# Optimization experiments

Hardware: AMD Instinct MI355X
Metric: run time of the kernel (lower is better)

Reference implementation:

```python
import jax, jax.numpy as jnp
import numpy as np

N = 100000   # nodes
E = 1600000  # edges (avg degree 16)
B = 64       # graphs in batch
D_IN = 64
D = 64       # d_model


def setup_inputs() -> dict:
    key = jax.random.key(0)
    ks = jax.random.split(key, 12)
    inp = {}
    inp["x_raw"] = jax.random.normal(ks[0], (N, D_IN), dtype=jnp.float32)
    inp["edge_index"] = jax.random.randint(ks[1], (2, E), 0, N)
    inp["batch"] = jnp.sort(jax.random.randint(ks[2], (N,), 0, B))
    # SAGEConv params per layer: lin_l (weight+bias, applied to neighbor mean),
    # lin_r (weight only, applied to root) -- PyG defaults.
    dins = [D_IN, D, D]
    for i, din in enumerate(dins):
        scale = 1.0 / np.sqrt(din)
        inp[f"Wl{i}"] = jax.random.normal(ks[3 + 3 * i], (D, din), dtype=jnp.float32) * scale
        inp[f"bl{i}"] = jnp.zeros((D,), dtype=jnp.float32)
        inp[f"Wr{i}"] = jax.random.normal(ks[4 + 3 * i], (D, din), dtype=jnp.float32) * scale
    return inp


def _sage_conv(x, src, dst, Wl, bl, Wr):
    """PyG SAGEConv(normalize=True): mean-aggregate neighbors, lin_l + lin_r, L2 norm."""
    msg = jax.ops.segment_sum(x[src], dst, num_segments=N)          # [N, d_in]
    deg = jax.ops.segment_sum(jnp.ones((src.shape[0],), x.dtype), dst, num_segments=N)
    mean = msg / jnp.maximum(deg, 1.0)[:, None]
    out = mean @ Wl.T + bl + x @ Wr.T                               # [N, D]
    nrm = jnp.sqrt(jnp.sum(out * out, axis=-1, keepdims=True))
    return out / jnp.maximum(nrm, 1e-12)


def reference(x_raw, edge_index, batch, Wl0, bl0, Wr0, Wl1, bl1, Wr1, Wl2, bl2, Wr2):
    src, dst = edge_index[0], edge_index[1]
    # dropout is identity in eval mode
    h = jax.nn.relu(_sage_conv(x_raw, src, dst, Wl0, bl0, Wr0))
    h = jax.nn.relu(_sage_conv(h, src, dst, Wl1, bl1, Wr1))
    h = jax.nn.relu(_sage_conv(h, src, dst, Wl2, bl2, Wr2))
    # readout='sum': scatter-sum over batch ids -> [B, D]
    return jax.ops.segment_sum(h, batch, num_segments=B)
```

## Files before the change

kernel.cpp:

```cpp
#include <hip/hip_runtime.h>

#define DFEAT 64

typedef __attribute__((ext_vector_type(8))) short bf16x8;
typedef __attribute__((ext_vector_type(4))) float f32x4;

__device__ __forceinline__ float bfhi(unsigned int u) {
    return __builtin_bit_cast(float, u & 0xFFFF0000u);
}
__device__ __forceinline__ float bflo(unsigned int u) {
    return __builtin_bit_cast(float, u << 16);
}
__device__ __forceinline__ unsigned short f2bf(float f) {
    unsigned int u = __builtin_bit_cast(unsigned int, f);
    u += 0x7FFFu + ((u >> 16) & 1u);
    return (unsigned short)(u >> 16);
}
__device__ __forceinline__ float4 upk4(uint2 v) {
    float4 r;
    r.x = bflo(v.x); r.y = bfhi(v.x);
    r.z = bflo(v.y); r.w = bfhi(v.y);
    return r;
}

__global__ void __launch_bounds__(256)
cvt_bf16_kernel(const float* __restrict__ in, unsigned short* __restrict__ outb,
                int n4) {
    int i = blockIdx.x * 256 + threadIdx.x;
    if (i >= n4) return;
    const float4 v = reinterpret_cast<const float4*>(in)[i];
    uint2 p;
    p.x = (unsigned int)f2bf(v.x) | ((unsigned int)f2bf(v.y) << 16);
    p.y = (unsigned int)f2bf(v.z) | ((unsigned int)f2bf(v.w) << 16);
    reinterpret_cast<uint2*>(outb)[i] = p;
}


__global__ void __launch_bounds__(256)
bucket_hist_kernel(const int* __restrict__ dsts, int* __restrict__ bhist, int E) {
    __shared__ int h[512];
    const int tid = threadIdx.x;
    h[tid] = 0; h[tid + 256] = 0;
    __syncthreads();
    for (int e = blockIdx.x * 256 + tid; e < E; e += gridDim.x * 256)
        atomicAdd(&h[dsts[e] >> 8], 1);
    __syncthreads();
    for (int b = tid; b < 512; b += 256)
        if (h[b]) atomicAdd(&bhist[b], h[b]);
}

__global__ void __launch_bounds__(256)
bucket_scan_kernel(const int* __restrict__ bhist, int* __restrict__ bbase,
                   int* __restrict__ bcur) {
    __shared__ int sm[512];
    const int tid = threadIdx.x;
    sm[tid] = bhist[tid]; sm[tid + 256] = bhist[tid + 256];
    __syncthreads();
    for (int s = 1; s < 512; s <<= 1) {
        int a0 = (tid >= s) ? sm[tid - s] : 0;
        int a1 = sm[tid + 256 - s];
        __syncthreads();
        sm[tid] += a0; sm[tid + 256] += a1;
        __syncthreads();
    }
    for (int b = tid; b < 512; b += 256) {
        int excl = b ? sm[b - 1] : 0;
        bbase[b] = excl; bcur[b] = excl;
    }
    if (tid == 0) bbase[512] = sm[511];
}

#define BIN_CH 2048
__global__ void __launch_bounds__(256)
bin_kernel(const int* __restrict__ srcs, const int* __restrict__ dsts,
           int* __restrict__ bcur, unsigned int* __restrict__ pairbuf, int E) {
    __shared__ int hist[512];
    __shared__ int sscan[512];
    __shared__ int gbase[512];
    __shared__ unsigned int staged[BIN_CH];
    __shared__ unsigned short sbkt[BIN_CH];

    const int tid = threadIdx.x;
    const int base = blockIdx.x * BIN_CH;
    const int chcnt = min(BIN_CH, E - base);

    hist[tid] = 0; hist[tid + 256] = 0;
    __syncthreads();

    unsigned int pk[8];
    unsigned short bb[8], rr[8];
#pragma unroll
    for (int k = 0; k < 8; ++k) {
        int i = k * 256 + tid;
        if (i < chcnt) {
            int e = base + i;
            int d = dsts[e];
            int s = srcs[e];
            int b = d >> 8;
            int r = atomicAdd(&hist[b], 1);
            pk[k] = ((unsigned int)(d & 255) << 24) | (unsigned int)s;
            bb[k] = (unsigned short)b;
            rr[k] = (unsigned short)r;
        } else {
            bb[k] = 0xFFFFu;
        }
    }
    __syncthreads();

    sscan[tid] = hist[tid]; sscan[tid + 256] = hist[tid + 256];
    __syncthreads();
    for (int s = 1; s < 512; s <<= 1) {
        int a0 = (tid >= s) ? sscan[tid - s] : 0;
        int a1 = sscan[tid + 256 - s];
        __syncthreads();
        sscan[tid] += a0; sscan[tid + 256] += a1;
        __syncthreads();
    }

    for (int b = tid; b < 512; b += 256) {
        int c = hist[b];
        gbase[b] = c ? atomicAdd(&bcur[b], c) : 0;
    }
    __syncthreads();

#pragma unroll
    for (int k = 0; k < 8; ++k) {
        if (bb[k] != 0xFFFFu) {
            int b = bb[k];
            int lpos = (b ? sscan[b - 1] : 0) + rr[k];
            staged[lpos] = pk[k];
            sbkt[lpos] = (unsigned short)b;
        }
    }
    __syncthreads();

    for (int i = tid; i < chcnt; i += 256) {
        int b = sbkt[i];
        int excl = b ? sscan[b - 1] : 0;
        pairbuf[gbase[b] + (i - excl)] = staged[i];
    }
}

__global__ void __launch_bounds__(256)
bucket_fill_kernel(const unsigned int* __restrict__ pairbuf,
                   const int* __restrict__ bbase,
                   int* __restrict__ rowptr, int* __restrict__ col,
                   int N, int E) {
    __shared__ int hist[256];
    __shared__ int scan_[256];
    __shared__ int cur[256];

    const int tid = threadIdx.x;
    const int b = blockIdx.x;
    const int node0 = b << 8;
    const int bb0 = bbase[b];
    const int cnt = bbase[b + 1] - bb0;

    hist[tid] = 0;
    __syncthreads();
    for (int i = tid; i < cnt; i += 256)
        atomicAdd(&hist[pairbuf[bb0 + i] >> 24], 1);
    __syncthreads();

    scan_[tid] = hist[tid];
    __syncthreads();
    for (int s = 1; s < 256; s <<= 1) {
        int a = (tid >= s) ? scan_[tid - s] : 0;
        __syncthreads();
        scan_[tid] += a;
        __syncthreads();
    }
    int excl = tid ? scan_[tid - 1] : 0;
    if (node0 + tid < N) rowptr[node0 + tid] = bb0 + excl;
    if (b == 0 && tid == 0) rowptr[N] = E;
    cur[tid] = bb0 + excl;
    __syncthreads();

    for (int i = tid; i < cnt; i += 256) {
        unsigned int p = pairbuf[bb0 + i];
        int pos = atomicAdd(&cur[p >> 24], 1);
        col[pos] = (int)(p & 0xFFFFFFu);
    }
}

__global__ void __launch_bounds__(256)
gather_mean_kernel(const unsigned short* __restrict__ xb,
                   const int* __restrict__ rowptr, const int* __restrict__ col,
                   unsigned short* __restrict__ meanb, int N) {
    int w = (blockIdx.x * 256 + threadIdx.x) >> 6;
    if (w >= N) return;
    const int lane = threadIdx.x & 63;
    const int r = lane >> 4;
    const int c = lane & 15;
    const uint2* x2 = reinterpret_cast<const uint2*>(xb);
    uint2* mean2 = reinterpret_cast<uint2*>(meanb);

    int st = rowptr[w], en = rowptr[w + 1];
    int deg = en - st;

    if (deg == 0) {
        if (r == 0) mean2[(size_t)w * 16 + c] = make_uint2(0, 0);
        return;
    }

    int nb = col[st + min(lane, deg - 1)];
    float4 acc = make_float4(0, 0, 0, 0);

#pragma unroll
    for (int k = 0; k < 4; ++k) {
        int i = 4 * k + r;
        int q = __shfl(nb, min(i, deg - 1), 64);
        float4 v = upk4(x2[(size_t)q * 16 + c]);
        float m = (i < deg) ? 1.0f : 0.0f;
        acc.x += v.x * m; acc.y += v.y * m; acc.z += v.z * m; acc.w += v.w * m;
    }
    if (deg > 16) {
#pragma unroll
        for (int k = 4; k < 8; ++k) {
            int i = 4 * k + r;
            int q = __shfl(nb, min(i, deg - 1), 64);
            float4 v = upk4(x2[(size_t)q * 16 + c]);
            float m = (i < deg) ? 1.0f : 0.0f;
            acc.x += v.x * m; acc.y += v.y * m; acc.z += v.z * m; acc.w += v.w * m;
        }
    }
    if (deg > 32) {
#pragma unroll
        for (int k = 8; k < 16; ++k) {
            int i = 4 * k + r;
            int q = __shfl(nb, min(i, deg - 1), 64);
            float4 v = upk4(x2[(size_t)q * 16 + c]);
            float m = (i < deg) ? 1.0f : 0.0f;
            acc.x += v.x * m; acc.y += v.y * m; acc.z += v.z * m; acc.w += v.w * m;
        }
    }
    for (int base = 64; base < deg; base += 64) {
        int cnt = deg - base;
        int nb2 = col[st + base + min(lane, cnt - 1)];
#pragma unroll
        for (int k = 0; k < 16; ++k) {
            int i = 4 * k + r;
            int q = __shfl(nb2, min(i, cnt - 1), 64);
            float4 v = upk4(x2[(size_t)q * 16 + c]);
            float m = (i < cnt) ? 1.0f : 0.0f;
            acc.x += v.x * m; acc.y += v.y * m; acc.z += v.z * m; acc.w += v.w * m;
        }
    }

#pragma unroll
    for (int off = 16; off <= 32; off <<= 1) {
        acc.x += __shfl_xor(acc.x, off, 64);
        acc.y += __shfl_xor(acc.y, off, 64);
        acc.z += __shfl_xor(acc.z, off, 64);
        acc.w += __shfl_xor(acc.w, off, 64);
    }
    float inv = 1.0f / (float)deg;
    if (r == 0) {
        uint2 p;
        p.x = (unsigned int)f2bf(acc.x * inv) | ((unsigned int)f2bf(acc.y * inv) << 16);
        p.y = (unsigned int)f2bf(acc.z * inv) | ((unsigned int)f2bf(acc.w * inv) << 16);
        mean2[(size_t)w * 16 + c] = p;
    }
}

__global__ void __launch_bounds__(256, 4)
transform_mfma_kernel(const unsigned short* __restrict__ xb,
                      const unsigned short* __restrict__ meanb,
                      const float* __restrict__ Wl, const float* __restrict__ bl,
                      const float* __restrict__ Wr,
                      unsigned short* __restrict__ h_out,
                      const int* __restrict__ batch, float* __restrict__ out,
                      int n_nodes, int final_layer) {
    __shared__ __align__(16) unsigned short Wlds[8192];

    const int tid = threadIdx.x;

    for (int i4 = tid; i4 < 1024; i4 += 256) {
        const float4 wl = reinterpret_cast<const float4*>(Wl)[i4];
        const float4 wr = reinterpret_cast<const float4*>(Wr)[i4];
        const int feat = i4 >> 4;
        const int n = feat >> 4, cc = feat & 15;
        const int k0 = (i4 & 15) << 2;
        const int qq = (k0 >> 3) & 3, tl = k0 >> 5, j0 = k0 & 7;
        const int lofs = (qq * 16 + cc) * 8 + j0;
        unsigned short* d0 = &Wlds[(n * 4 + tl) * 512 + lofs];
        d0[0] = f2bf(wl.x); d0[1] = f2bf(wl.y); d0[2] = f2bf(wl.z); d0[3] = f2bf(wl.w);
        unsigned short* d1 = &Wlds[(n * 4 + 2 + tl) * 512 + lofs];
        d1[0] = f2bf(wr.x); d1[1] = f2bf(wr.y); d1[2] = f2bf(wr.z); d1[3] = f2bf(wr.w);
    }
    __syncthreads();

    const int tiles = (n_nodes + 15) >> 4;
    const int tile = blockIdx.x * 4 + (tid >> 6);
    if (tile >= tiles) return;

    const int lane = tid & 63;
    const int c = lane & 15;
    const int q = lane >> 4;
    const bf16x8* fragp = reinterpret_cast<const bf16x8*>(Wlds);

    const int base = tile << 4;
    const int nodeB = min(base + c, n_nodes - 1);
    const bool valid = (base + c) < n_nodes;

    const uint4* mrow = reinterpret_cast<const uint4*>(&meanb[(size_t)nodeB * 64]);
    const uint4* xrow = reinterpret_cast<const uint4*>(&xb[(size_t)nodeB * 64]);
    bf16x8 F0 = __builtin_bit_cast(bf16x8, mrow[q]);
    bf16x8 F1 = __builtin_bit_cast(bf16x8, mrow[4 + q]);
    bf16x8 F2 = __builtin_bit_cast(bf16x8, xrow[q]);
    bf16x8 F3 = __builtin_bit_cast(bf16x8, xrow[4 + q]);

    f32x4 acc[4];
#pragma unroll
    for (int n = 0; n < 4; ++n) acc[n] = (f32x4){0.f, 0.f, 0.f, 0.f};

#pragma unroll
    for (int n = 0; n < 4; ++n) {
        bf16x8 w0 = fragp[(n * 4 + 0) * 64 + lane];
        bf16x8 w1 = fragp[(n * 4 + 1) * 64 + lane];
        bf16x8 w2 = fragp[(n * 4 + 2) * 64 + lane];
        bf16x8 w3 = fragp[(n * 4 + 3) * 64 + lane];
        acc[n] = __builtin_amdgcn_mfma_f32_16x16x32_bf16(w0, F0, acc[n], 0, 0, 0);
        acc[n] = __builtin_amdgcn_mfma_f32_16x16x32_bf16(w1, F1, acc[n], 0, 0, 0);
        acc[n] = __builtin_amdgcn_mfma_f32_16x16x32_bf16(w2, F2, acc[n], 0, 0, 0);
        acc[n] = __builtin_amdgcn_mfma_f32_16x16x32_bf16(w3, F3, acc[n], 0, 0, 0);
    }

    float v[4][4];
    float ss = 0.f;
#pragma unroll
    for (int n = 0; n < 4; ++n) {
        const float4 b4 = reinterpret_cast<const float4*>(bl)[n * 4 + q];
        v[n][0] = acc[n][0] + b4.x;
        v[n][1] = acc[n][1] + b4.y;
        v[n][2] = acc[n][2] + b4.z;
        v[n][3] = acc[n][3] + b4.w;
#pragma unroll
        for (int r = 0; r < 4; ++r) ss += v[n][r] * v[n][r];
    }
    ss += __shfl_xor(ss, 16, 64);
    ss += __shfl_xor(ss, 32, 64);
    const float inv = 1.0f / fmaxf(sqrtf(ss), 1e-12f);

    if (!final_layer) {
        if (valid) {
            uint2* dst = reinterpret_cast<uint2*>(&h_out[(size_t)(base + c) * 64]);
#pragma unroll
            for (int n = 0; n < 4; ++n) {
                float o0 = fmaxf(v[n][0] * inv, 0.f), o1 = fmaxf(v[n][1] * inv, 0.f);
                float o2 = fmaxf(v[n][2] * inv, 0.f), o3 = fmaxf(v[n][3] * inv, 0.f);
                uint2 p;
                p.x = (unsigned int)f2bf(o0) | ((unsigned int)f2bf(o1) << 16);
                p.y = (unsigned int)f2bf(o2) | ((unsigned int)f2bf(o3) << 16);
                dst[n * 4 + q] = p;
            }
        }
    } else {
        float o[4][4];
#pragma unroll
        for (int n = 0; n < 4; ++n)
#pragma unroll
            for (int r = 0; r < 4; ++r)
                o[n][r] = valid ? fmaxf(v[n][r] * inv, 0.f) : 0.f;

        const int lastn = min(base + 15, n_nodes - 1);
        const int gb0 = batch[base];
        if (gb0 == batch[lastn]) {
#pragma unroll
            for (int n = 0; n < 4; ++n)
#pragma unroll
                for (int r = 0; r < 4; ++r) {
                    float s = o[n][r];
                    s += __shfl_xor(s, 1, 64);
                    s += __shfl_xor(s, 2, 64);
                    s += __shfl_xor(s, 4, 64);
                    s += __shfl_xor(s, 8, 64);
                    if (c == 0)
                        atomicAdd(&out[(size_t)gb0 * DFEAT + n * 16 + q * 4 + r], s);
                }
        } else {
            if (valid) {
                const int gb = batch[base + c];
#pragma unroll
                for (int n = 0; n < 4; ++n)
#pragma unroll
                    for (int r = 0; r < 4; ++r)
                        atomicAdd(&out[(size_t)gb * DFEAT + n * 16 + q * 4 + r], o[n][r]);
            }
        }
    }
}

extern "C" void kernel_launch(void* const* d_in, const int* in_sizes, int n_in,
                              void* d_out, int out_size, void* d_ws, size_t ws_size,
                              hipStream_t stream) {
    const float* x_raw = (const float*)d_in[0];
    const int*   eidx  = (const int*)d_in[1];
    const int*   batch = (const int*)d_in[2];
    const float* Wl0 = (const float*)d_in[3];
    const float* bl0 = (const float*)d_in[4];
    const float* Wr0 = (const float*)d_in[5];
    const float* Wl1 = (const float*)d_in[6];
    const float* bl1 = (const float*)d_in[7];
    const float* Wr1 = (const float*)d_in[8];
    const float* Wl2 = (const float*)d_in[9];
    const float* bl2 = (const float*)d_in[10];
    const float* Wr2 = (const float*)d_in[11];

    const int N = in_sizes[0] / DFEAT;
    const int E = in_sizes[1] / 2;
    const int* srcs = eidx;
    const int* dsts = eidx + E;
    float* out = (float*)d_out;

    const int NB = (N + 255) >> 8;

    char* ws = (char*)d_ws;
    auto align512 = [](size_t v) { return (v + 511) & ~(size_t)511; };
    size_t off = 0;
    int* rowptr = (int*)(ws + off); off += align512(((size_t)N + 1) * 4);
    int* col    = (int*)(ws + off); off += align512((size_t)E * 4);
    int* bhist  = (int*)(ws + off); off += align512(512 * 4);
    int* bbase  = (int*)(ws + off); off += align512(513 * 4);
    int* bcur   = (int*)(ws + off); off += align512(512 * 4);
    unsigned short* xb    = (unsigned short*)(ws + off); off += align512((size_t)N * DFEAT * 2);
    unsigned short* meanb = (unsigned short*)(ws + off); off += align512((size_t)N * DFEAT * 2);
    unsigned short* hA    = (unsigned short*)(ws + off); off += align512((size_t)N * DFEAT * 2);
    unsigned short* hB    = (unsigned short*)(ws + off);
    unsigned int* pairbuf = (unsigned int*)hA;

    hipMemsetAsync(bhist, 0, 512 * 4, stream);
    hipMemsetAsync(out, 0, (size_t)out_size * 4, stream);

    const int n4 = N * DFEAT / 4;
    cvt_bf16_kernel<<<(n4 + 255) / 256, 256, 0, stream>>>(x_raw, xb, n4);

    bucket_hist_kernel<<<512, 256, 0, stream>>>(dsts, bhist, E);
    bucket_scan_kernel<<<1, 256, 0, stream>>>(bhist, bbase, bcur);
    bin_kernel<<<(E + BIN_CH - 1) / BIN_CH, 256, 0, stream>>>(srcs, dsts, bcur, pairbuf, E);
    bucket_fill_kernel<<<NB, 256, 0, stream>>>(pairbuf, bbase, rowptr, col, N, E);

    const int gatherBlocks = (N + 3) / 4;
    const int tiles    = (N + 15) / 16;
    const int xfBlocks = (tiles + 3) / 4;

    gather_mean_kernel<<<gatherBlocks, 256, 0, stream>>>(xb, rowptr, col, meanb, N);
    transform_mfma_kernel<<<xfBlocks, 256, 0, stream>>>(xb, meanb, Wl0, bl0, Wr0,
                                                        hA, nullptr, nullptr, N, 0);
    gather_mean_kernel<<<gatherBlocks, 256, 0, stream>>>(hA, rowptr, col, meanb, N);
    transform_mfma_kernel<<<xfBlocks, 256, 0, stream>>>(hA, meanb, Wl1, bl1, Wr1,
                                                        hB, nullptr, nullptr, N, 0);
    gather_mean_kernel<<<gatherBlocks, 256, 0, stream>>>(hB, rowptr, col, meanb, N);
    transform_mfma_kernel<<<xfBlocks, 256, 0, stream>>>(hB, meanb, Wl2, bl2, Wr2,
                                                        nullptr, batch, out, N, 1);
}
```

Baseline: 342.4 us.

## Fuse neighbor mean gather into MFMA transform kernel per SAGE layer

Removes the separate gather_mean kernel and meanb buffer; each lane of the MFMA transform kernel now serially walks its own node's neighbor list, loading 16-byte row chunks with one-step software prefetch, and builds the mean fragment in registers. This drops a global write and read of the mean tensor and three kernel launches. In exchange, the gather becomes a per-node serial loop with 4 lanes per node instead of a whole wavefront per node, so there is less memory-level parallelism and wavefronts diverge on uneven degrees.

```diff
diff --git a/kernel.cpp b/kernel.cpp
--- a/kernel.cpp
+++ b/kernel.cpp
@@ -15,12 +15,6 @@
     unsigned int u = __builtin_bit_cast(unsigned int, f);
     u += 0x7FFFu + ((u >> 16) & 1u);
     return (unsigned short)(u >> 16);
-}
-__device__ __forceinline__ float4 upk4(uint2 v) {
-    float4 r;
-    r.x = bflo(v.x); r.y = bfhi(v.x);
-    r.z = bflo(v.y); r.w = bfhi(v.y);
-    return r;
 }
 
 __global__ void __launch_bounds__(256)
@@ -183,94 +177,14 @@
     }
 }
 
-__global__ void __launch_bounds__(256)
-gather_mean_kernel(const unsigned short* __restrict__ xb,
-                   const int* __restrict__ rowptr, const int* __restrict__ col,
-                   unsigned short* __restrict__ meanb, int N) {
-    int w = (blockIdx.x * 256 + threadIdx.x) >> 6;
-    if (w >= N) return;
-    const int lane = threadIdx.x & 63;
-    const int r = lane >> 4;
-    const int c = lane & 15;
-    const uint2* x2 = reinterpret_cast<const uint2*>(xb);
-    uint2* mean2 = reinterpret_cast<uint2*>(meanb);
-
-    int st = rowptr[w], en = rowptr[w + 1];
-    int deg = en - st;
-
-    if (deg == 0) {
-        if (r == 0) mean2[(size_t)w * 16 + c] = make_uint2(0, 0);
-        return;
-    }
-
-    int nb = col[st + min(lane, deg - 1)];
-    float4 acc = make_float4(0, 0, 0, 0);
-
-#pragma unroll
-    for (int k = 0; k < 4; ++k) {
-        int i = 4 * k + r;
-        int q = __shfl(nb, min(i, deg - 1), 64);
-        float4 v = upk4(x2[(size_t)q * 16 + c]);
-        float m = (i < deg) ? 1.0f : 0.0f;
-        acc.x += v.x * m; acc.y += v.y * m; acc.z += v.z * m; acc.w += v.w * m;
-    }
-    if (deg > 16) {
-#pragma unroll
-        for (int k = 4; k < 8; ++k) {
-            int i = 4 * k + r;
-            int q = __shfl(nb, min(i, deg - 1), 64);
-            float4 v = upk4(x2[(size_t)q * 16 + c]);
-            float m = (i < deg) ? 1.0f : 0.0f;
-            acc.x += v.x * m; acc.y += v.y * m; acc.z += v.z * m; acc.w += v.w * m;
-        }
-    }
-    if (deg > 32) {
-#pragma unroll
-        for (int k = 8; k < 16; ++k) {
-            int i = 4 * k + r;
-            int q = __shfl(nb, min(i, deg - 1), 64);
-            float4 v = upk4(x2[(size_t)q * 16 + c]);
-            float m = (i < deg) ? 1.0f : 0.0f;
-            acc.x += v.x * m; acc.y += v.y * m; acc.z += v.z * m; acc.w += v.w * m;
-        }
-    }
-    for (int base = 64; base < deg; base += 64) {
-        int cnt = deg - base;
-        int nb2 = col[st + base + min(lane, cnt - 1)];
-#pragma unroll
-        for (int k = 0; k < 16; ++k) {
-            int i = 4 * k + r;
-            int q = __shfl(nb2, min(i, cnt - 1), 64);
-            float4 v = upk4(x2[(size_t)q * 16 + c]);
-            float m = (i < cnt) ? 1.0f : 0.0f;
-            acc.x += v.x * m; acc.y += v.y * m; acc.z += v.z * m; acc.w += v.w * m;
-        }
-    }
-
-#pragma unroll
-    for (int off = 16; off <= 32; off <<= 1) {
-        acc.x += __shfl_xor(acc.x, off, 64);
-        acc.y += __shfl_xor(acc.y, off, 64);
-        acc.z += __shfl_xor(acc.z, off, 64);
-        acc.w += __shfl_xor(acc.w, off, 64);
-    }
-    float inv = 1.0f / (float)deg;
-    if (r == 0) {
-        uint2 p;
-        p.x = (unsigned int)f2bf(acc.x * inv) | ((unsigned int)f2bf(acc.y * inv) << 16);
-        p.y = (unsigned int)f2bf(acc.z * inv) | ((unsigned int)f2bf(acc.w * inv) << 16);
-        mean2[(size_t)w * 16 + c] = p;
-    }
-}
-
 __global__ void __launch_bounds__(256, 4)
-transform_mfma_kernel(const unsigned short* __restrict__ xb,
-                      const unsigned short* __restrict__ meanb,
-                      const float* __restrict__ Wl, const float* __restrict__ bl,
-                      const float* __restrict__ Wr,
-                      unsigned short* __restrict__ h_out,
-                      const int* __restrict__ batch, float* __restrict__ out,
-                      int n_nodes, int final_layer) {
+fused_sage_kernel(const unsigned short* __restrict__ xb,
+                  const int* __restrict__ rowptr, const int* __restrict__ col,
+                  const float* __restrict__ Wl, const float* __restrict__ bl,
+                  const float* __restrict__ Wr,
+                  unsigned short* __restrict__ h_out,
+                  const int* __restrict__ batch, float* __restrict__ out,
+                  int n_nodes, int final_layer) {
     __shared__ __align__(16) unsigned short Wlds[8192];
 
     const int tid = threadIdx.x;
@@ -300,15 +214,48 @@
     const bf16x8* fragp = reinterpret_cast<const bf16x8*>(Wlds);
 
     const int base = tile << 4;
-    const int nodeB = min(base + c, n_nodes - 1);
     const bool valid = (base + c) < n_nodes;
-
-    const uint4* mrow = reinterpret_cast<const uint4*>(&meanb[(size_t)nodeB * 64]);
-    const uint4* xrow = reinterpret_cast<const uint4*>(&xb[(size_t)nodeB * 64]);
-    bf16x8 F0 = __builtin_bit_cast(bf16x8, mrow[q]);
-    bf16x8 F1 = __builtin_bit_cast(bf16x8, mrow[4 + q]);
-    bf16x8 F2 = __builtin_bit_cast(bf16x8, xrow[q]);
-    bf16x8 F3 = __builtin_bit_cast(bf16x8, xrow[4 + q]);
+    const int node = valid ? (base + c) : (n_nodes - 1);
+
+    const uint4* rows4 = reinterpret_cast<const uint4*>(xb);
+    const int st = rowptr[node];
+    const int deg = valid ? (rowptr[node + 1] - st) : 0;
+
+    float accA[8], accB[8];
+#pragma unroll
+    for (int j = 0; j < 8; ++j) { accA[j] = 0.f; accB[j] = 0.f; }
+
+    if (deg > 0) {
+        int nbB = col[st];
+        uint4 a0 = rows4[(size_t)nbB * 8 + q];
+        uint4 b0 = rows4[(size_t)nbB * 8 + 4 + q];
+        nbB = col[st + min(1, deg - 1)];
+        for (int j = 0; j < deg; ++j) {
+            const int nbC = col[st + min(j + 2, deg - 1)];
+            const uint4 a1 = rows4[(size_t)nbB * 8 + q];
+            const uint4 b1 = rows4[(size_t)nbB * 8 + 4 + q];
+            accA[0] += bflo(a0.x); accA[1] += bfhi(a0.x);
+            accA[2] += bflo(a0.y); accA[3] += bfhi(a0.y);
+            accA[4] += bflo(a0.z); accA[5] += bfhi(a0.z);
+            accA[6] += bflo(a0.w); accA[7] += bfhi(a0.w);
+            accB[0] += bflo(b0.x); accB[1] += bfhi(b0.x);
+            accB[2] += bflo(b0.y); accB[3] += bfhi(b0.y);
+            accB[4] += bflo(b0.z); accB[5] += bfhi(b0.z);
+            accB[6] += bflo(b0.w); accB[7] += bfhi(b0.w);
+            a0 = a1; b0 = b1; nbB = nbC;
+        }
+    }
+
+    const float inv = (deg > 0) ? (1.0f / (float)deg) : 0.0f;
+    bf16x8 F0, F1;
+#pragma unroll
+    for (int j = 0; j < 8; ++j) {
+        F0[j] = (short)f2bf(accA[j] * inv);
+        F1[j] = (short)f2bf(accB[j] * inv);
+    }
+    const uint4* xrow = reinterpret_cast<const uint4*>(&xb[(size_t)node * 64]);
+    const bf16x8 F2 = __builtin_bit_cast(bf16x8, xrow[q]);
+    const bf16x8 F3 = __builtin_bit_cast(bf16x8, xrow[4 + q]);
 
     f32x4 acc[4];
 #pragma unroll
@@ -340,15 +287,15 @@
     }
     ss += __shfl_xor(ss, 16, 64);
     ss += __shfl_xor(ss, 32, 64);
-    const float inv = 1.0f / fmaxf(sqrtf(ss), 1e-12f);
+    const float nrm = 1.0f / fmaxf(sqrtf(ss), 1e-12f);
 
     if (!final_layer) {
         if (valid) {
             uint2* dst = reinterpret_cast<uint2*>(&h_out[(size_t)(base + c) * 64]);
 #pragma unroll
             for (int n = 0; n < 4; ++n) {
-                float o0 = fmaxf(v[n][0] * inv, 0.f), o1 = fmaxf(v[n][1] * inv, 0.f);
-                float o2 = fmaxf(v[n][2] * inv, 0.f), o3 = fmaxf(v[n][3] * inv, 0.f);
+                float o0 = fmaxf(v[n][0] * nrm, 0.f), o1 = fmaxf(v[n][1] * nrm, 0.f);
+                float o2 = fmaxf(v[n][2] * nrm, 0.f), o3 = fmaxf(v[n][3] * nrm, 0.f);
                 uint2 p;
                 p.x = (unsigned int)f2bf(o0) | ((unsigned int)f2bf(o1) << 16);
                 p.y = (unsigned int)f2bf(o2) | ((unsigned int)f2bf(o3) << 16);
@@ -361,7 +308,7 @@
         for (int n = 0; n < 4; ++n)
 #pragma unroll
             for (int r = 0; r < 4; ++r)
-                o[n][r] = valid ? fmaxf(v[n][r] * inv, 0.f) : 0.f;
+                o[n][r] = valid ? fmaxf(v[n][r] * nrm, 0.f) : 0.f;
 
         const int lastn = min(base + 15, n_nodes - 1);
         const int gb0 = batch[base];
@@ -423,10 +370,9 @@
     int* bhist  = (int*)(ws + off); off += align512(512 * 4);
     int* bbase  = (int*)(ws + off); off += align512(513 * 4);
     int* bcur   = (int*)(ws + off); off += align512(512 * 4);
-    unsigned short* xb    = (unsigned short*)(ws + off); off += align512((size_t)N * DFEAT * 2);
-    unsigned short* meanb = (unsigned short*)(ws + off); off += align512((size_t)N * DFEAT * 2);
-    unsigned short* hA    = (unsigned short*)(ws + off); off += align512((size_t)N * DFEAT * 2);
-    unsigned short* hB    = (unsigned short*)(ws + off);
+    unsigned short* xb = (unsigned short*)(ws + off); off += align512((size_t)N * DFEAT * 2);
+    unsigned short* hA = (unsigned short*)(ws + off); off += align512((size_t)N * DFEAT * 2);
+    unsigned short* hB = (unsigned short*)(ws + off);
     unsigned int* pairbuf = (unsigned int*)hA;
 
     hipMemsetAsync(bhist, 0, 512 * 4, stream);
@@ -440,17 +386,13 @@
     bin_kernel<<<(E + BIN_CH - 1) / BIN_CH, 256, 0, stream>>>(srcs, dsts, bcur, pairbuf, E);
     bucket_fill_kernel<<<NB, 256, 0, stream>>>(pairbuf, bbase, rowptr, col, N, E);
 
-    const int gatherBlocks = (N + 3) / 4;
     const int tiles    = (N + 15) / 16;
     const int xfBlocks = (tiles + 3) / 4;
 
-    gather_mean_kernel<<<gatherBlocks, 256, 0, stream>>>(xb, rowptr, col, meanb, N);
-    transform_mfma_kernel<<<xfBlocks, 256, 0, stream>>>(xb, meanb, Wl0, bl0, Wr0,
-                                                        hA, nullptr, nullptr, N, 0);
-    gather_mean_kernel<<<gatherBlocks, 256, 0, stream>>>(hA, rowptr, col, meanb, N);
-    transform_mfma_kernel<<<xfBlocks, 256, 0, stream>>>(hA, meanb, Wl1, bl1, Wr1,
-                                                        hB, nullptr, nullptr, N, 0);
-    gather_mean_kernel<<<gatherBlocks, 256, 0, stream>>>(hB, rowptr, col, meanb, N);
-    transform_mfma_kernel<<<xfBlocks, 256, 0, stream>>>(hB, meanb, Wl2, bl2, Wr2,
-                                                        nullptr, batch, out, N, 1);
-}
+    fused_sage_kernel<<<xfBlocks, 256, 0, stream>>>(xb, rowptr, col, Wl0, bl0, Wr0,
+                                                    hA, nullptr, nullptr, N, 0);
+    fused_sage_kernel<<<xfBlocks, 256, 0, stream>>>(hA, rowptr, col, Wl1, bl1, Wr1,
+                                                    hB, nullptr, nullptr, N, 0);
+    fused_sage_kernel<<<xfBlocks, 256, 0, stream>>>(hB, rowptr, col, Wl2, bl2, Wr2,
+                                                    nullptr, batch, out, N, 1);
+}
```

After: 315.3 us. -7.9%, faster.
